# Kernel tuning notes

Measured on AMD Instinct MI355X. Metric: run time of the kernel, lower is better.

The kernel has to match this reference:

```python
import jax, jax.numpy as jnp
import numpy as np

B, N, IN_DIM, EMB, HEADS, M, ITERS = 8, 4096, 1024, 512, 4, 256, 6
DH = EMB // HEADS
SCALE = DH ** -0.5
RES_K = 33  # residual depthwise conv kernel size (TransMIL / nystrom-attention default)


def setup_inputs() -> dict:
    key = jax.random.key(0)
    ks = iter(jax.random.split(key, 40))
    def rn(shape, s=0.02):
        return jax.random.normal(next(ks), shape, jnp.float32) * s
    inp = {"X": jax.random.normal(next(ks), (B, N, IN_DIM), jnp.float32)}
    inp["few_w"] = rn((IN_DIM, EMB)); inp["few_b"] = jnp.zeros((EMB,), jnp.float32)
    inp["cls_token"] = rn((1, 1, EMB), 1.0)
    for i in (1, 2):
        inp[f"l{i}_ln_g"] = jnp.ones((EMB,), jnp.float32)
        inp[f"l{i}_ln_b"] = jnp.zeros((EMB,), jnp.float32)
        inp[f"l{i}_qkv_w"] = rn((EMB, 3 * EMB))
        inp[f"l{i}_out_w"] = rn((EMB, EMB))
        inp[f"l{i}_out_b"] = jnp.zeros((EMB,), jnp.float32)
        inp[f"l{i}_res_k"] = rn((HEADS, 1, RES_K, 1))
    for ksz in (7, 5, 3):
        inp[f"ppeg_k{ksz}"] = rn((EMB, 1, ksz, ksz))
        inp[f"ppeg_b{ksz}"] = jnp.zeros((EMB,), jnp.float32)
    inp["norm_g"] = jnp.ones((EMB,), jnp.float32)
    inp["norm_b"] = jnp.zeros((EMB,), jnp.float32)
    inp["cls_w"] = rn((EMB, 1)); inp["cls_b"] = jnp.zeros((1,), jnp.float32)
    return inp


def _ln(x, g, b):
    mu = x.mean(-1, keepdims=True)
    var = x.var(-1, keepdims=True)
    return (x - mu) / jnp.sqrt(var + 1e-5) * g + b


def _pinv(x, iters):
    # Moore-Penrose iterative pseudo-inverse of (..., m, m)
    abs_x = jnp.abs(x)
    z = jnp.swapaxes(x, -1, -2) / (abs_x.sum(-1).max() * abs_x.sum(-2).max())
    I = jnp.eye(x.shape[-1], dtype=x.dtype)
    for _ in range(iters):
        xz = x @ z
        z = 0.25 * z @ (13 * I - xz @ (15 * I - xz @ (7 * I - xz)))
    return z


def _nystrom_layer(x, ln_g, ln_b, qkv_w, out_w, out_b, res_k):
    # pre-norm transformer layer with Nystrom attention + residual depthwise conv
    b, n, d = x.shape
    h = _ln(x, ln_g, ln_b)
    pad = (-n) % M  # left-pad so seq divisible by n_landmarks
    hp = jnp.pad(h, ((0, 0), (pad, 0), (0, 0)))
    n_p = n + pad
    q, k, v = jnp.split(hp @ qkv_w, 3, axis=-1)
    def to_heads(t):
        return t.reshape(b, n_p, HEADS, DH).transpose(0, 2, 1, 3)  # (b,h,n,dh)
    q, k, v = to_heads(q) * SCALE, to_heads(k), to_heads(v)
    l = n_p // M
    q_l = q.reshape(b, HEADS, M, l, DH).mean(3)  # landmark means
    k_l = k.reshape(b, HEADS, M, l, DH).mean(3)
    a1 = jax.nn.softmax(jnp.einsum('bhid,bhjd->bhij', q, k_l), -1)    # (b,h,n,m)
    a2 = jax.nn.softmax(jnp.einsum('bhid,bhjd->bhij', q_l, k_l), -1)  # (b,h,m,m)
    a3 = jax.nn.softmax(jnp.einsum('bhid,bhjd->bhij', q_l, k), -1)    # (b,h,m,n)
    out = a1 @ (_pinv(a2, ITERS) @ (a3 @ v))
    # residual depthwise conv over sequence, one channel per head
    res = jax.lax.conv_general_dilated(
        v, res_k, (1, 1), ((RES_K // 2, RES_K // 2), (0, 0)),
        dimension_numbers=('NCHW', 'OIHW', 'NCHW'), feature_group_count=HEADS)
    out = out + res
    out = out.transpose(0, 2, 1, 3).reshape(b, n_p, d) @ out_w + out_b
    return x + out[:, -n:]


def _dwconv(x, k, bias, pad):
    y = jax.lax.conv_general_dilated(
        x, k, (1, 1), ((pad, pad), (pad, pad)),
        dimension_numbers=('NCHW', 'OIHW', 'NCHW'), feature_group_count=EMB)
    return y + bias[None, :, None, None]


def _ppeg(x, H, W, k7, b7, k5, b5, k3, b3):
    b, _, c = x.shape
    cls_t, feat = x[:, :1], x[:, 1:]
    f = feat.transpose(0, 2, 1).reshape(b, c, H, W)
    y = f + _dwconv(f, k7, b7, 3) + _dwconv(f, k5, b5, 2) + _dwconv(f, k3, b3, 1)
    y = y.reshape(b, c, H * W).transpose(0, 2, 1)
    return jnp.concatenate([cls_t, y], axis=1)


def _forward(X, few_w, few_b, cls_token,
             l1_ln_g, l1_ln_b, l1_qkv_w, l1_out_w, l1_out_b, l1_res_k,
             l2_ln_g, l2_ln_b, l2_qkv_w, l2_out_w, l2_out_b, l2_res_k,
             ppeg_k7, ppeg_b7, ppeg_k5, ppeg_b5, ppeg_k3, ppeg_b3,
             norm_g, norm_b, cls_w, cls_b):
    b, bag = X.shape[0], X.shape[1]
    h = X @ few_w + few_b
    ps = int(np.ceil(np.sqrt(bag)))
    add = ps * ps - bag
    h = jnp.concatenate([h, h[:, :add]], axis=1)  # pad bag to perfect square
    h = jnp.concatenate([jnp.broadcast_to(cls_token, (b, 1, EMB)), h], axis=1)
    h = _nystrom_layer(h, l1_ln_g, l1_ln_b, l1_qkv_w, l1_out_w, l1_out_b, l1_res_k)
    h = _ppeg(h, ps, ps, ppeg_k7, ppeg_b7, ppeg_k5, ppeg_b5, ppeg_k3, ppeg_b3)
    h = _nystrom_layer(h, l2_ln_g, l2_ln_b, l2_qkv_w, l2_out_w, l2_out_b, l2_res_k)
    h = _ln(h, norm_g, norm_b)
    return (h[:, 0] @ cls_w + cls_b).squeeze(-1)  # (batch,) bag logits


def reference(X, few_w, few_b, cls_token,
              l1_ln_g, l1_ln_b, l1_qkv_w, l1_out_w, l1_out_b, l1_res_k,
              l2_ln_g, l2_ln_b, l2_qkv_w, l2_out_w, l2_out_b, l2_res_k,
              ppeg_k7, ppeg_b7, ppeg_k5, ppeg_b5, ppeg_k3, ppeg_b3,
              norm_g, norm_b, cls_w, cls_b):
    return _forward(X, few_w, few_b, cls_token,
                    l1_ln_g, l1_ln_b, l1_qkv_w, l1_out_w, l1_out_b, l1_res_k,
                    l2_ln_g, l2_ln_b, l2_qkv_w, l2_out_w, l2_out_b, l2_res_k,
                    ppeg_k7, ppeg_b7, ppeg_k5, ppeg_b5, ppeg_k3, ppeg_b3,
                    norm_g, norm_b, cls_w, cls_b)
```

## Files before the change

### kernel.cpp

```cpp
#include <hip/hip_runtime.h>

constexpr int BATCH = 8;
constexpr int NTOK  = 4097;
constexpr int NP    = 4352;
constexpr int PADR  = 255;
constexpr int EMBD  = 512;
constexpr int DHD   = 128;
constexpr int LSUB  = 17;
constexpr float SCALE_F = 0.08838834764831845f;

constexpr int PPS   = 72;
constexpr int PPLN  = 72 * 70;
constexpr long long TPAD_FLOATS = (long long)BATCH * EMBD * PPLN;

typedef unsigned short u16;
typedef short   s16x8 __attribute__((ext_vector_type(8)));
typedef u16     u16x4 __attribute__((ext_vector_type(4)));
typedef float   f32x4 __attribute__((ext_vector_type(4)));

__device__ __forceinline__ u16 f2bf(float x) {
    unsigned u = __float_as_uint(x);
    u += 0x7fffu + ((u >> 16) & 1u);
    return (u16)(u >> 16);
}
__device__ __forceinline__ float bf2f(u16 h) {
    return __uint_as_float(((unsigned)h) << 16);
}

__device__ __forceinline__ void gload16(const u16* gp, u16* lp) {
    __builtin_amdgcn_global_load_lds(
        (const __attribute__((address_space(1))) unsigned int*)gp,
        (__attribute__((address_space(3))) unsigned int*)lp,
        16, 0, 0);
}

__device__ __forceinline__ float block_sum256(float v) {
    __shared__ float tmp[4];
    __syncthreads();
#pragma unroll
    for (int off = 32; off > 0; off >>= 1) v += __shfl_down(v, off, 64);
    int t = threadIdx.x;
    if ((t & 63) == 0) tmp[t >> 6] = v;
    __syncthreads();
    return tmp[0] + tmp[1] + tmp[2] + tmp[3];
}

__device__ __forceinline__ float block_max256(float v) {
    __shared__ float tmp[4];
    __syncthreads();
#pragma unroll
    for (int off = 32; off > 0; off >>= 1) v = fmaxf(v, __shfl_down(v, off, 64));
    int t = threadIdx.x;
    if ((t & 63) == 0) tmp[t >> 6] = v;
    __syncthreads();
    return fmaxf(fmaxf(tmp[0], tmp[1]), fmaxf(tmp[2], tmp[3]));
}

struct GemmP {
    const float* A; const float* B; float* C; const float* bias;
    long long As1, As2, Bs1, Bs2, Cs1, Cs2;
    int Adiv, Bdiv, Cdiv;
    int Am, Bk, Bn, Cm, Arow, Crow;
    int M, N, K, nb;
    float alpha; int accum;
    float bdiagc; int btrans; float cdiagc; int ctrans;
};

constexpr int LDSTR = 40;
constexpr int AH = 0, AL = 2560, BHs = 5120, BLs = 7680;

__global__ __launch_bounds__(256) void gemm_k(GemmP p) {
    __shared__ u16 lds[10240];
    const int bz = blockIdx.z;
    const float* Ab = p.A + (long long)(bz / p.Adiv) * p.As1 + (long long)(bz % p.Adiv) * p.As2;
    const float* Bb = p.B + (long long)(bz / p.Bdiv) * p.Bs1 + (long long)(bz % p.Bdiv) * p.Bs2;
    float*       Cb = p.C + (long long)(bz / p.Cdiv) * p.Cs1 + (long long)(bz % p.Cdiv) * p.Cs2;
    const int m0 = blockIdx.y * 64, n0 = blockIdx.x * 64;
    const int t = threadIdx.x;
    const int wave = t >> 6, lane = t & 63;
    const int wm = (wave & 1) * 32, wn = (wave >> 1) * 32;
    const int quad = lane >> 4, l15 = lane & 15;

    f32x4 acc[2][2];
#pragma unroll
    for (int i = 0; i < 2; ++i)
#pragma unroll
        for (int j = 0; j < 2; ++j) acc[i][j] = (f32x4){0.f, 0.f, 0.f, 0.f};

    for (int k0 = 0; k0 < p.K; k0 += 32) {
        {
            const int ar = t >> 2, ac = (t & 3) * 8;
            float v[8];
            if (m0 + ar < p.M) {
                const float* s = Ab + (long long)(m0 + ar + p.Arow) * p.Am + (k0 + ac);
                float4 x0 = *(const float4*)s, x1 = *(const float4*)(s + 4);
                v[0] = x0.x; v[1] = x0.y; v[2] = x0.z; v[3] = x0.w;
                v[4] = x1.x; v[5] = x1.y; v[6] = x1.z; v[7] = x1.w;
            } else {
#pragma unroll
                for (int i = 0; i < 8; ++i) v[i] = 0.f;
            }
            u16 h[8], l[8];
#pragma unroll
            for (int i = 0; i < 8; ++i) { h[i] = f2bf(v[i]); l[i] = f2bf(v[i] - bf2f(h[i])); }
            const int off = ar * LDSTR + ac;
            u16x4 a0, a1, b0, b1;
#pragma unroll
            for (int i = 0; i < 4; ++i) { a0[i] = h[i]; a1[i] = h[i + 4]; b0[i] = l[i]; b1[i] = l[i + 4]; }
            *(u16x4*)&lds[AH + off] = a0; *(u16x4*)&lds[AH + off + 4] = a1;
            *(u16x4*)&lds[AL + off] = b0; *(u16x4*)&lds[AL + off + 4] = b1;
        }
        if (p.Bn == 1) {
            const int bk = t >> 3, n8 = (t & 7) * 8;
            const float* s = Bb + (long long)(k0 + bk) * p.Bk + (n0 + n8);
            float4 x0 = *(const float4*)s, x1 = *(const float4*)(s + 4);
            float v[8] = {x0.x, x0.y, x0.z, x0.w, x1.x, x1.y, x1.z, x1.w};
            if (p.btrans) {
                const int gk = k0 + bk;
#pragma unroll
                for (int i = 0; i < 8; ++i)
                    v[i] = (gk == n0 + n8 + i ? p.bdiagc : 0.f) - v[i];
            }
#pragma unroll
            for (int i = 0; i < 8; ++i) {
                int j = (i + (t & 7)) & 7;
                u16 h = f2bf(v[j]);
                lds[BHs + (n8 + j) * LDSTR + bk] = h;
                lds[BLs + (n8 + j) * LDSTR + bk] = f2bf(v[j] - bf2f(h));
            }
        } else {
            const int bn = t >> 2, k8 = (t & 3) * 8;
            const float* s = Bb + (long long)(n0 + bn) * p.Bn + (k0 + k8);
            float4 x0 = *(const float4*)s, x1 = *(const float4*)(s + 4);
            float v[8] = {x0.x, x0.y, x0.z, x0.w, x1.x, x1.y, x1.z, x1.w};
            u16 h[8], l[8];
#pragma unroll
            for (int i = 0; i < 8; ++i) { h[i] = f2bf(v[i]); l[i] = f2bf(v[i] - bf2f(h[i])); }
            const int off = bn * LDSTR + k8;
            u16x4 a0, a1, b0, b1;
#pragma unroll
            for (int i = 0; i < 4; ++i) { a0[i] = h[i]; a1[i] = h[i + 4]; b0[i] = l[i]; b1[i] = l[i + 4]; }
            *(u16x4*)&lds[BHs + off] = a0; *(u16x4*)&lds[BHs + off + 4] = a1;
            *(u16x4*)&lds[BLs + off] = b0; *(u16x4*)&lds[BLs + off + 4] = b1;
        }
        __syncthreads();

        s16x8 ah[2], al[2], bh[2], bl[2];
#pragma unroll
        for (int mi = 0; mi < 2; ++mi) {
            const int off = (wm + mi * 16 + l15) * LDSTR + quad * 8;
            u16x4 q0 = *(const u16x4*)&lds[AH + off], q1 = *(const u16x4*)&lds[AH + off + 4];
            u16x4 r0 = *(const u16x4*)&lds[AL + off], r1 = *(const u16x4*)&lds[AL + off + 4];
            s16x8 fh, fl;
#pragma unroll
            for (int i = 0; i < 4; ++i) { fh[i] = q0[i]; fh[i + 4] = q1[i]; fl[i] = r0[i]; fl[i + 4] = r1[i]; }
            ah[mi] = fh; al[mi] = fl;
        }
#pragma unroll
        for (int ni = 0; ni < 2; ++ni) {
            const int off = (wn + ni * 16 + l15) * LDSTR + quad * 8;
            u16x4 q0 = *(const u16x4*)&lds[BHs + off], q1 = *(const u16x4*)&lds[BHs + off + 4];
            u16x4 r0 = *(const u16x4*)&lds[BLs + off], r1 = *(const u16x4*)&lds[BLs + off + 4];
            s16x8 fh, fl;
#pragma unroll
            for (int i = 0; i < 4; ++i) { fh[i] = q0[i]; fh[i + 4] = q1[i]; fl[i] = r0[i]; fl[i + 4] = r1[i]; }
            bh[ni] = fh; bl[ni] = fl;
        }
#pragma unroll
        for (int mi = 0; mi < 2; ++mi)
#pragma unroll
            for (int ni = 0; ni < 2; ++ni) {
                acc[mi][ni] = __builtin_amdgcn_mfma_f32_16x16x32_bf16(ah[mi], bh[ni], acc[mi][ni], 0, 0, 0);
                acc[mi][ni] = __builtin_amdgcn_mfma_f32_16x16x32_bf16(ah[mi], bl[ni], acc[mi][ni], 0, 0, 0);
                acc[mi][ni] = __builtin_amdgcn_mfma_f32_16x16x32_bf16(al[mi], bh[ni], acc[mi][ni], 0, 0, 0);
            }
        __syncthreads();
    }

#pragma unroll
    for (int mi = 0; mi < 2; ++mi)
#pragma unroll
        for (int ni = 0; ni < 2; ++ni) {
            const int n = n0 + wn + ni * 16 + l15;
#pragma unroll
            for (int r = 0; r < 4; ++r) {
                const int m = m0 + wm + mi * 16 + quad * 4 + r;
                if (m >= p.M) continue;
                float v = p.alpha * acc[mi][ni][r];
                if (p.bias) v += p.bias[n];
                if (p.ctrans) v = (m == n ? p.cdiagc : 0.f) - v;
                float* dst = Cb + (long long)(m + p.Crow) * p.Cm + n;
                if (p.accum) *dst += v; else *dst = v;
            }
        }
}

struct SplitP {
    const float* src; u16* dh; u16* dl;
    long long s1, s2, rstride, dstride, total;
    int div, R, C8;
    float scale;
};
__global__ __launch_bounds__(256) void split_k(SplitP p) {
    long long idx = (long long)blockIdx.x * 256 + threadIdx.x;
    if (idx >= p.total) return;
    int c8 = (int)(idx % p.C8);
    long long tmp = idx / p.C8;
    int r  = (int)(tmp % p.R);
    int bz = (int)(tmp / p.R);
    const float* s = p.src + (long long)(bz / p.div) * p.s1 + (long long)(bz % p.div) * p.s2
                   + (long long)r * p.rstride + c8 * 8;
    float4 x0 = *(const float4*)s, x1 = *(const float4*)(s + 4);
    float v[8] = {x0.x, x0.y, x0.z, x0.w, x1.x, x1.y, x1.z, x1.w};
    s16x8 hv, lv;
#pragma unroll
    for (int i = 0; i < 8; ++i) {
        float sv = v[i] * p.scale;
        u16 h = f2bf(sv);
        hv[i] = (short)h;
        lv[i] = (short)f2bf(sv - bf2f(h));
    }
    long long doff = (long long)bz * p.dstride + (long long)r * (p.C8 * 8) + c8 * 8;
    *(s16x8*)&p.dh[doff] = hv;
    *(s16x8*)&p.dl[doff] = lv;
}

__global__ __launch_bounds__(256) void splitT_k(const float* __restrict__ src,
                                                u16* __restrict__ dh, u16* __restrict__ dl,
                                                int K, int N) {
    int idx = blockIdx.x * 256 + threadIdx.x;
    if (idx >= N * K) return;
    int n = idx / K, k = idx - n * K;
    float v = src[(long long)k * N + n];
    u16 h = f2bf(v);
    dh[idx] = h;
    dl[idx] = f2bf(v - bf2f(h));
}

struct GemmBtP {
    const u16 *Ah, *Al, *Bh, *Bl;
    float* C; const float* bias;
    long long Abs, Bbs, Cbs;
    int M, N, K, Cm, Crow, accum;
};

__global__ __launch_bounds__(512, 4) void gemm_bt_k(GemmBtP p) {
    __shared__ __align__(16) u16 lds[16384];
    const int bz = blockIdx.z;
    const u16* Ahb = p.Ah + (long long)bz * p.Abs;
    const u16* Alb = p.Al + (long long)bz * p.Abs;
    const u16* Bhb = p.Bh + (long long)bz * p.Bbs;
    const u16* Blb = p.Bl + (long long)bz * p.Bbs;
    float*     Cb  = p.C  + (long long)bz * p.Cbs;

    const int NX = gridDim.x;
    const int nwg = NX * gridDim.y;
    const int bid = blockIdx.y * NX + blockIdx.x;
    const int qq = nwg >> 3, rr = nwg & 7;
    const int xcd = bid & 7, loc = bid >> 3;
    const int nbid = (xcd < rr) ? (xcd * (qq + 1) + loc)
                                : (rr * (qq + 1) + (xcd - rr) * qq + loc);
    const int m0 = (nbid / NX) * 128, n0 = (nbid % NX) * 256;

    const int t = threadIdx.x;
    const int wave = t >> 6, lane = t & 63;
    const int wm = (wave & 1) * 64, wn = (wave >> 1) * 64;
    const int quad = lane >> 4, l15 = lane & 15;
    const int K = p.K;

    const int srow = 16 * wave + (lane >> 2);
    const int sga  = (m0 + srow < p.M) ? (m0 + srow) : (p.M - 1);
    const long long sbase = (long long)sga * K + (lane & 3) * 8;
    u16* ldsw = &lds[wave * 512];

    const long long bb0   = (long long)(n0 + wn + l15) * K + quad * 8;
    const long long bstep = 16LL * K;

    f32x4 acc[4][4];
#pragma unroll
    for (int i = 0; i < 4; ++i)
#pragma unroll
        for (int j = 0; j < 4; ++j) acc[i][j] = (f32x4){0.f, 0.f, 0.f, 0.f};

    gload16(Ahb + sbase, ldsw);
    gload16(Alb + sbase, ldsw + 4096);
    __syncthreads();

    const int nt = K >> 5;
    int cur = 0;
    for (int t0 = 0; t0 < nt; ++t0) {
        const int k0 = t0 << 5;
        s16x8 bh[4], bl[4];
#pragma unroll
        for (int ni = 0; ni < 4; ++ni) {
            const long long bo = bb0 + ni * bstep + k0;
            bh[ni] = *(const s16x8*)&Bhb[bo];
            bl[ni] = *(const s16x8*)&Blb[bo];
        }
        if (t0 + 1 < nt) {
            u16* dst = ldsw + (cur ^ 1) * 8192;
            gload16(Ahb + sbase + k0 + 32, dst);
            gload16(Alb + sbase + k0 + 32, dst + 4096);
        }
        const int bufo = cur * 8192;
#pragma unroll
        for (int mi = 0; mi < 4; ++mi) {
            const int off = bufo + (wm + mi * 16 + l15) * 32 + quad * 8;
            s16x8 ah = *(const s16x8*)&lds[off];
            s16x8 al = *(const s16x8*)&lds[off + 4096];
#pragma unroll
            for (int ni = 0; ni < 4; ++ni) {
                acc[mi][ni] = __builtin_amdgcn_mfma_f32_16x16x32_bf16(ah, bh[ni], acc[mi][ni], 0, 0, 0);
                acc[mi][ni] = __builtin_amdgcn_mfma_f32_16x16x32_bf16(ah, bl[ni], acc[mi][ni], 0, 0, 0);
                acc[mi][ni] = __builtin_amdgcn_mfma_f32_16x16x32_bf16(al, bh[ni], acc[mi][ni], 0, 0, 0);
            }
        }
        __syncthreads();
        cur ^= 1;
    }

#pragma unroll
    for (int mi = 0; mi < 4; ++mi)
#pragma unroll
        for (int ni = 0; ni < 4; ++ni) {
            const int n = n0 + wn + ni * 16 + l15;
            const float bv = p.bias ? p.bias[n] : 0.f;
#pragma unroll
            for (int r = 0; r < 4; ++r) {
                const int m = m0 + wm + mi * 16 + quad * 4 + r;
                if (m >= p.M) continue;
                float* dst = Cb + (long long)(m + p.Crow) * p.Cm + n;
                float v = acc[mi][ni][r] + bv;
                if (p.accum) *dst += v; else *dst = v;
            }
        }
}

__global__ void cls_set_k(float* H0, const float* cls) {
    int t = blockIdx.x * 256 + threadIdx.x;
    int b = t >> 9, c = t & 511;
    H0[(long long)b * NTOK * EMBD + c] = cls[c];
}

__global__ __launch_bounds__(256) void ln_pad_k(const float* __restrict__ H0,
                                                u16* __restrict__ oh, u16* __restrict__ ol,
                                                const float* g, const float* bb) {
    int row = blockIdx.x, b = blockIdx.y, t = threadIdx.x;
    long long off = ((long long)b * NP + row) * EMBD;
    if (row < PADR) {
        oh[off + t] = 0; oh[off + t + 256] = 0;
        ol[off + t] = 0; ol[off + t + 256] = 0;
        return;
    }
    const float* x = H0 + ((long long)b * NTOK + (row - PADR)) * EMBD;
    float v0 = x[t], v1 = x[t + 256];
    float mu = block_sum256(v0 + v1) * (1.f / EMBD);
    float d0 = v0 - mu, d1 = v1 - mu;
    float var = block_sum256(d0 * d0 + d1 * d1) * (1.f / EMBD);
    float rs = 1.f / sqrtf(var + 1e-5f);
    float y0 = d0 * rs * g[t]       + bb[t];
    float y1 = d1 * rs * g[t + 256] + bb[t + 256];
    u16 h0 = f2bf(y0); oh[off + t]       = h0; ol[off + t]       = f2bf(y0 - bf2f(h0));
    u16 h1 = f2bf(y1); oh[off + t + 256] = h1; ol[off + t + 256] = f2bf(y1 - bf2f(h1));
}

__global__ void landmark_k(const float* __restrict__ QKV, float* __restrict__ QL,
                           float* __restrict__ KL) {
    long long idx = (long long)blockIdx.x * 256 + threadIdx.x;
    int d = idx & 127; int i = (int)((idx >> 7) & 255); int bh = (int)(idx >> 15);
    int b = bh >> 2, h = bh & 3;
    const float* base = QKV + (long long)b * NP * 1536 + (long long)i * LSUB * 1536 + h * DHD + d;
    float sq = 0.f, sk = 0.f;
#pragma unroll
    for (int j = 0; j < LSUB; ++j) { sq += base[j * 1536]; sk += base[j * 1536 + EMBD]; }
    QL[idx] = sq * (1.f / LSUB);
    KL[idx] = sk * (1.f / LSUB);
}

__global__ __launch_bounds__(256) void softmax256_k(float* __restrict__ X) {
    long long row = (long long)blockIdx.x * 4 + (threadIdx.x >> 6);
    int lane = threadIdx.x & 63;
    float4* p = (float4*)(X + row * 256) + lane;
    float4 v = *p;
    float m = fmaxf(fmaxf(v.x, v.y), fmaxf(v.z, v.w));
#pragma unroll
    for (int off = 32; off > 0; off >>= 1) m = fmaxf(m, __shfl_xor(m, off, 64));
    float ex = __expf(v.x - m), ey = __expf(v.y - m), ez = __expf(v.z - m), ew = __expf(v.w - m);
    float s = ex + ey + ez + ew;
#pragma unroll
    for (int off = 32; off > 0; off >>= 1) s += __shfl_xor(s, off, 64);
    float inv = 1.f / s;
    *p = make_float4(ex * inv, ey * inv, ez * inv, ew * inv);
}

__global__ __launch_bounds__(256) void softmax_k(float* __restrict__ X, int L) {
    float4* p = (float4*)(X + (long long)blockIdx.x * L);
    int nv = L >> 2, t = threadIdx.x;
    float m = -1e30f;
    for (int i = t; i < nv; i += 256) {
        float4 v = p[i];
        m = fmaxf(m, fmaxf(fmaxf(v.x, v.y), fmaxf(v.z, v.w)));
    }
    m = block_max256(m);
    float s = 0.f;
    for (int i = t; i < nv; i += 256) {
        float4 v = p[i];
        v.x = __expf(v.x - m); v.y = __expf(v.y - m); v.z = __expf(v.z - m); v.w = __expf(v.w - m);
        p[i] = v;
        s += v.x + v.y + v.z + v.w;
    }
    s = block_sum256(s);
    float inv = 1.f / s;
    for (int i = t; i < nv; i += 256) {
        float4 v = p[i];
        p[i] = make_float4(v.x * inv, v.y * inv, v.z * inv, v.w * inv);
    }
}

__global__ __launch_bounds__(256) void pinv_absmax_k(const float* __restrict__ X, float* red) {
    int bh = blockIdx.x, t = threadIdx.x;
    const float* x = X + (long long)bh * 65536;
    float rs = 0.f, cs = 0.f;
    for (int j = 0; j < 256; ++j) { rs += fabsf(x[t * 256 + j]); cs += fabsf(x[j * 256 + t]); }
    float mr = block_max256(rs);
    float mc = block_max256(cs);
    if (t == 0) { red[bh] = mr; red[32 + bh] = mc; }
}

__global__ void pinv_scalar_k(const float* red, float* inv) {
    float mr = 0.f, mc = 0.f;
    for (int i = 0; i < 32; ++i) { mr = fmaxf(mr, red[i]); mc = fmaxf(mc, red[32 + i]); }
    inv[0] = 1.f / (mr * mc);
}

__global__ void pinv_tinit_k(const float* __restrict__ X, const float* __restrict__ inv,
                             float* __restrict__ Z) {
    long long idx = (long long)blockIdx.x * 256 + threadIdx.x;
    int j = (int)(idx & 255); int i = (int)((idx >> 8) & 255); long long bh = idx >> 16;
    Z[idx] = X[(bh << 16) + ((long long)j << 8) + i] * inv[0];
}

__global__ void resconv_k(const float* __restrict__ QKV, const float* __restrict__ rk,
                          float* __restrict__ ATT2) {
    long long idx = (long long)blockIdx.x * 256 + threadIdx.x;
    if (idx >= (long long)BATCH * NTOK * EMBD) return;
    int c = (int)(idx & 511); long long r = idx >> 9;
    int n = PADR + (int)(r % NTOK); int b = (int)(r / NTOK);
    int h = c >> 7, d = c & 127;
    const float* vb = QKV + (long long)b * NP * 1536 + 1024 + h * DHD + d;
    float acc = 0.f;
#pragma unroll
    for (int u = 0; u < 33; ++u) {
        int nn = n + u - 16;
        if (nn >= 0 && nn < NP) acc += vb[(long long)nn * 1536] * rk[h * 33 + u];
    }
    ATT2[((long long)b * NP + n) * EMBD + c] += acc;
}

__global__ void wsum_k(const float* __restrict__ k7, const float* __restrict__ k5,
                       const float* __restrict__ k3, const float* __restrict__ b7,
                       const float* __restrict__ b5, const float* __restrict__ b3,
                       float* __restrict__ W) {
    int idx = blockIdx.x * 256 + threadIdx.x;
    if (idx < 25088) {
        int c = idx / 49, i = idx - c * 49;
        int dy = i / 7, dx = i - dy * 7;
        float w = k7[idx];
        if (dy >= 1 && dy <= 5 && dx >= 1 && dx <= 5) w += k5[c * 25 + (dy - 1) * 5 + (dx - 1)];
        if (dy >= 2 && dy <= 4 && dx >= 2 && dx <= 4) w += k3[c * 9 + (dy - 2) * 3 + (dx - 2)];
        W[idx] = w;
    } else if (idx < 25600) {
        int c = idx - 25088;
        W[25088 + c] = b7[c] + b5[c] + b3[c];
    }
}

__global__ __launch_bounds__(256) void tin_k(const float* __restrict__ H0,
                                             float* __restrict__ Tpad) {
    __shared__ float lds[64][65];
    const int y = blockIdx.x, c0 = blockIdx.y * 64, b = blockIdx.z;
    const int t = threadIdx.x;
    const int pc = t & 63, pr4 = t >> 6;
    const float* src = H0 + ((long long)b * NTOK + 1 + y * 64) * EMBD + c0;
#pragma unroll
    for (int i = 0; i < 16; ++i) {
        int pr = pr4 + i * 4;
        lds[pr][pc] = src[(long long)pr * EMBD + pc];
    }
    __syncthreads();
    const int xw = t & 63, cw4 = t >> 6;
#pragma unroll
    for (int i = 0; i < 16; ++i) {
        int cw = cw4 + i * 4;
        Tpad[(long long)(b * 512 + c0 + cw) * PPLN + (3 + y) * PPS + 3 + xw] = lds[xw][cw];
    }
}

__global__ __launch_bounds__(256, 4) void conv7_k(const float* __restrict__ Tpad,
                                                  const float* __restrict__ Wall,
                                                  float* __restrict__ Tout) {
    const int bc = blockIdx.x;
    const int c = bc & 511;
    const int t = threadIdx.x;
    const int x = t & 63, band = t >> 6;
    const int y0 = band * 16;
    const float* in = Tpad + (long long)bc * PPLN + x;
    float* outp = Tout + (long long)bc * 4096 + x;

    float W[49];
#pragma unroll
    for (int i = 0; i < 49; ++i) W[i] = Wall[c * 49 + i];
    const float bias = Wall[25088 + c];

    float win[7][7];
#pragma unroll
    for (int j = 0; j < 6; ++j)
#pragma unroll
        for (int d = 0; d < 7; ++d)
            win[j][d] = in[(y0 + j) * PPS + d];

#pragma unroll
    for (int yy = 0; yy < 16; ++yy) {
        const int slot = (6 + yy) % 7;
#pragma unroll
        for (int d = 0; d < 7; ++d)
            win[slot][d] = in[(y0 + yy + 6) * PPS + d];
        float s = bias + win[(yy + 3) % 7][3];
#pragma unroll
        for (int dy = 0; dy < 7; ++dy) {
            const int r = (yy + dy) % 7;
#pragma unroll
            for (int dx = 0; dx < 7; ++dx)
                s += W[dy * 7 + dx] * win[r][dx];
        }
        outp[(y0 + yy) * 64] = s;
    }
}

__global__ __launch_bounds__(256) void tout_k(const float* __restrict__ Tout,
                                              float* __restrict__ H0) {
    __shared__ float lds[64][65];
    const int y = blockIdx.x, c0 = blockIdx.y * 64, b = blockIdx.z;
    const int t = threadIdx.x;
    const int xl = t & 63, cl4 = t >> 6;
#pragma unroll
    for (int i = 0; i < 16; ++i) {
        int cl = cl4 + i * 4;
        lds[xl][cl] = Tout[(long long)(b * 512 + c0 + cl) * 4096 + y * 64 + xl];
    }
    __syncthreads();
    const int pc = t & 63, pl4 = t >> 6;
    float* dst = H0 + ((long long)b * NTOK + 1 + y * 64) * EMBD + c0;
#pragma unroll
    for (int i = 0; i < 16; ++i) {
        int pl = pl4 + i * 4;
        dst[(long long)pl * EMBD + pc] = lds[pl][pc];
    }
}

__global__ __launch_bounds__(256) void head_k(const float* __restrict__ H0, const float* g,
                                              const float* bb, const float* cw, const float* cb,
                                              float* __restrict__ out) {
    int b = blockIdx.x, t = threadIdx.x;
    const float* x = H0 + (long long)b * NTOK * EMBD;
    float v0 = x[t], v1 = x[t + 256];
    float mu = block_sum256(v0 + v1) * (1.f / EMBD);
    float d0 = v0 - mu, d1 = v1 - mu;
    float var = block_sum256(d0 * d0 + d1 * d1) * (1.f / EMBD);
    float rs = 1.f / sqrtf(var + 1e-5f);
    float y0 = d0 * rs * g[t] + bb[t];
    float y1 = d1 * rs * g[t + 256] + bb[t + 256];
    float s = block_sum256(y0 * cw[t] + y1 * cw[t + 256]);
    if (t == 0) out[b] = s + cb[0];
}

extern "C" void kernel_launch(void* const* d_in, const int* in_sizes, int n_in,
                              void* d_out, int out_size, void* d_ws, size_t ws_size,
                              hipStream_t stream) {
    (void)in_sizes; (void)n_in; (void)out_size; (void)ws_size;
    const float* X        = (const float*)d_in[0];
    const float* few_w    = (const float*)d_in[1];
    const float* few_b    = (const float*)d_in[2];
    const float* cls_tok  = (const float*)d_in[3];
    const float* ln_g[2]  = {(const float*)d_in[4],  (const float*)d_in[10]};
    const float* ln_b[2]  = {(const float*)d_in[5],  (const float*)d_in[11]};
    const float* qkv_w[2] = {(const float*)d_in[6],  (const float*)d_in[12]};
    const float* out_w[2] = {(const float*)d_in[7],  (const float*)d_in[13]};
    const float* out_b[2] = {(const float*)d_in[8],  (const float*)d_in[14]};
    const float* res_k[2] = {(const float*)d_in[9],  (const float*)d_in[15]};
    const float* k7 = (const float*)d_in[16]; const float* b7 = (const float*)d_in[17];
    const float* k5 = (const float*)d_in[18]; const float* b5 = (const float*)d_in[19];
    const float* k3 = (const float*)d_in[20]; const float* b3 = (const float*)d_in[21];
    const float* norm_g = (const float*)d_in[22]; const float* norm_b = (const float*)d_in[23];
    const float* cls_w  = (const float*)d_in[24]; const float* cls_b  = (const float*)d_in[25];
    float* out = (float*)d_out;

    float* ws  = (float*)d_ws;
    float* H0  = ws;
    float* LNH = H0  + 16781312LL;
    float* QKV = LNH + 17825792LL;
    float* A3  = QKV + 53477376LL;
    float* QL  = A3  + 35651584LL;
    float* KL  = QL  + 1048576LL;
    float* A2  = KL  + 1048576LL;
    float* KV  = A2  + 2097152LL;
    float* ZKV = KV  + 1048576LL;
    float* RED = ZKV + 1048576LL;

    u16* LNHh = (u16*)LNH;
    u16* LNHl = (u16*)(LNH + 8912896LL);
    u16* QLh  = (u16*)KV;
    u16* QLl  = (u16*)(KV + 524288LL);
    u16* KLh  = (u16*)ZKV;
    u16* KLl  = (u16*)(ZKV + 524288LL);
    u16* Xh   = (u16*)A3;
    u16* Xl   = (u16*)(A3 + 16777216LL);
    u16* ATh  = (u16*)A3;
    u16* ATl  = (u16*)(A3 + 8390656LL);
    u16* Wh   = (u16*)A2;
    u16* fwl  = (u16*)(A2 + 262144LL);
    u16* qwl  = (u16*)(A2 + 393216LL);
    u16* owl  = (u16*)(A2 + 131072LL);
    float* Zb0 = LNH;
    float* Zb1 = LNH + 2097152LL;
    float* XZm = LNH + 4194304LL;
    float* U1  = LNH + 6291456LL;
    float* U2  = LNH + 8388608LL;
    float* Tpad = QKV;
    float* Tout = QKV + TPAD_FLOATS;
    float* WSUM = A3;

    auto gemmx = [&](const float* A, long long As1, long long As2, int Adiv, int Am, int Arow,
                     const float* Bm, long long Bs1, long long Bs2, int Bdiv, int Bk, int Bn,
                     float* C, long long Cs1, long long Cs2, int Cdiv, int Cm, int Crow,
                     int M, int N, int K, int nb, float alpha, int accum, const float* bias,
                     float bdiagc, int btrans, float cdiagc, int ctrans) {
        GemmP p;
        p.A = A; p.B = Bm; p.C = C; p.bias = bias;
        p.As1 = As1; p.As2 = As2; p.Bs1 = Bs1; p.Bs2 = Bs2; p.Cs1 = Cs1; p.Cs2 = Cs2;
        p.Adiv = Adiv; p.Bdiv = Bdiv; p.Cdiv = Cdiv;
        p.Am = Am; p.Bk = Bk; p.Bn = Bn; p.Cm = Cm; p.Arow = Arow; p.Crow = Crow;
        p.M = M; p.N = N; p.K = K; p.nb = nb; p.alpha = alpha; p.accum = accum;
        p.bdiagc = bdiagc; p.btrans = btrans; p.cdiagc = cdiagc; p.ctrans = ctrans;
        dim3 grid(N / 64, (M + 63) / 64, nb);
        gemm_k<<<grid, 256, 0, stream>>>(p);
    };
    auto gemm = [&](const float* A, long long As1, long long As2, int Adiv, int Am, int Arow,
                    const float* Bm, long long Bs1, long long Bs2, int Bdiv, int Bk, int Bn,
                    float* C, long long Cs1, long long Cs2, int Cdiv, int Cm, int Crow,
                    int M, int N, int K, int nb, float alpha, int accum, const float* bias) {
        gemmx(A, As1, As2, Adiv, Am, Arow, Bm, Bs1, Bs2, Bdiv, Bk, Bn,
              C, Cs1, Cs2, Cdiv, Cm, Crow, M, N, K, nb, alpha, accum, bias, 0.f, 0, 0.f, 0);
    };
    auto split = [&](const float* src, u16* dh, u16* dl, long long s1, long long s2, int div,
                     long long rstride, int R, int C, int nb, float scale) {
        SplitP p;
        p.src = src; p.dh = dh; p.dl = dl;
        p.s1 = s1; p.s2 = s2; p.div = div;
        p.rstride = rstride; p.R = R; p.C8 = C >> 3;
        p.dstride = (long long)R * C;
        p.total = (long long)nb * R * (C >> 3);
        p.scale = scale;
        int blocks = (int)((p.total + 255) / 256);
        split_k<<<blocks, 256, 0, stream>>>(p);
    };
    auto gemmbt = [&](const u16* Ah, const u16* Al, long long Abs,
                      const u16* Bh, const u16* Bl, long long Bbs,
                      float* C, long long Cbs, int Cm, int Crow,
                      int M, int N, int K, int nb, int accum, const float* bias) {
        GemmBtP p;
        p.Ah = Ah; p.Al = Al; p.Bh = Bh; p.Bl = Bl;
        p.C = C; p.bias = bias;
        p.Abs = Abs; p.Bbs = Bbs; p.Cbs = Cbs;
        p.M = M; p.N = N; p.K = K; p.Cm = Cm; p.Crow = Crow; p.accum = accum;
        dim3 grid(N / 256, (M + 127) / 128, nb);
        gemm_bt_k<<<grid, 512, 0, stream>>>(p);
    };

    cls_set_k<<<16, 256, 0, stream>>>(H0, cls_tok);
    split(X, Xh, Xl, 0, 0, 1, 1024, 32768, 1024, 1, 1.f);
    splitT_k<<<2048, 256, 0, stream>>>(few_w, Wh, fwl, 1024, 512);
    gemmbt(Xh, Xl, 4194304LL, Wh, fwl, 0,
           H0, 2097664LL, 512, 1,
           4096, 512, 1024, BATCH, 0, few_b);

    for (int L = 0; L < 2; ++L) {
        ln_pad_k<<<dim3(NP, BATCH), 256, 0, stream>>>(H0, LNHh, LNHl, ln_g[L], ln_b[L]);
        splitT_k<<<3072, 256, 0, stream>>>(qkv_w[L], Wh, qwl, 512, 1536);
        gemmbt(LNHh, LNHl, 0, Wh, qwl, 0,
               QKV, 0, 1536, 0,
               34816, 1536, 512, 1, 0, nullptr);
        landmark_k<<<4096, 256, 0, stream>>>(QKV, QL, KL);
        gemm(QL, 32768LL, 0, 1, 128, 0,
             KL, 32768LL, 0, 1, 1, 128,
             A2, 65536LL, 0, 1, 256, 0,
             256, 256, 128, 32, SCALE_F, 0, nullptr);
        softmax256_k<<<2048, 256, 0, stream>>>(A2);
        split(QL, QLh, QLl, 32768LL, 0, 1, 128, 256, 128, 32, SCALE_F);
        split(KL, KLh, KLl, 32768LL, 0, 1, 128, 256, 128, 32, 1.f);
        split(QKV + 512, LNHh, LNHl, 6680064LL, 128LL, 4, 1536, 4352, 128, 32, 1.f);
        gemmbt(QLh, QLl, 32768LL, LNHh, LNHl, 557056LL,
               A3, 1114112LL, 4352, 0,
               256, 4352, 128, 32, 0, nullptr);
        softmax_k<<<8192, 256, 0, stream>>>(A3, 4352);
        gemm(A3, 1114112LL, 0, 1, 4352, 0,
             QKV + 1024, 6680064LL, 128LL, 4, 1536, 1,
             KV, 32768LL, 0, 1, 128, 0,
             256, 128, 4352, 32, 1.f, 0, nullptr);
        split(QKV, LNHh, LNHl, 6680064LL, 128LL, 4, 1536, 4352, 128, 32, SCALE_F);
        gemmbt(LNHh, LNHl, 557056LL, KLh, KLl, 32768LL,
               A3, 1114112LL, 256, 0,
               4352, 256, 128, 32, 0, nullptr);
        softmax256_k<<<34816, 256, 0, stream>>>(A3);
        pinv_absmax_k<<<32, 256, 0, stream>>>(A2, RED);
        pinv_scalar_k<<<1, 1, 0, stream>>>(RED, RED + 64);
        pinv_tinit_k<<<8192, 256, 0, stream>>>(A2, RED + 64, Zb0);
        float* zc = Zb0; float* zn = Zb1;
        for (int it = 0; it < 6; ++it) {
            gemm(A2, 65536LL, 0, 1, 256, 0, zc, 65536LL, 0, 1, 256, 1,
                 XZm, 65536LL, 0, 1, 256, 0, 256, 256, 256, 32, 1.f, 0, nullptr);
            gemmx(XZm, 65536LL, 0, 1, 256, 0, XZm, 65536LL, 0, 1, 256, 1,
                  U1, 65536LL, 0, 1, 256, 0, 256, 256, 256, 32, 1.f, 0, nullptr,
                  7.f, 1, 15.f, 1);
            gemmx(XZm, 65536LL, 0, 1, 256, 0, U1, 65536LL, 0, 1, 256, 1,
                  U2, 65536LL, 0, 1, 256, 0, 256, 256, 256, 32, 1.f, 0, nullptr,
                  0.f, 0, 13.f, 1);
            gemm(zc, 65536LL, 0, 1, 256, 0, U2, 65536LL, 0, 1, 256, 1,
                 zn, 65536LL, 0, 1, 256, 0, 256, 256, 256, 32, 0.25f, 0, nullptr);
            float* t2 = zc; zc = zn; zn = t2;
        }
        gemm(zc, 65536LL, 0, 1, 256, 0,
             KV, 32768LL, 0, 1, 128, 1,
             ZKV, 32768LL, 0, 1, 128, 0,
             256, 128, 256, 32, 1.f, 0, nullptr);
        gemm(A3, 1114112LL, 0, 1, 256, 0,
             ZKV, 32768LL, 0, 1, 128, 1,
             LNH, 2228224LL, 128LL, 4, 512, 0,
             4352, 128, 256, 32, 1.f, 0, nullptr);
        resconv_k<<<65552, 256, 0, stream>>>(QKV, res_k[L], LNH);
        split(LNH + PADR * 512, ATh, ATl, 2228224LL, 0, 1, 512, 4097, 512, 8, 1.f);
        splitT_k<<<1024, 256, 0, stream>>>(out_w[L], Wh, owl, 512, 512);
        gemmbt(ATh, ATl, 2097664LL, Wh, owl, 0,
               H0, 2097664LL, 512, 0,
               4097, 512, 512, BATCH, 1, out_b[L]);

        if (L == 0) {
            hipMemsetAsync(Tpad, 0, TPAD_FLOATS * sizeof(float), stream);
            wsum_k<<<101, 256, 0, stream>>>(k7, k5, k3, b7, b5, b3, WSUM);
            tin_k<<<dim3(64, 8, 8), 256, 0, stream>>>(H0, Tpad);
            conv7_k<<<4096, 256, 0, stream>>>(Tpad, WSUM, Tout);
            tout_k<<<dim3(64, 8, 8), 256, 0, stream>>>(Tout, H0);
        }
    }

    head_k<<<BATCH, 256, 0, stream>>>(H0, norm_g, norm_b, cls_w, cls_b, out);
}
```

Measured before the change: 4.372 ms.

## Deepen gemm_bt K-tile to 64 with XOR-swizzled LDS; cache softmax rows in LDS

The split-bf16 GEMM (B-transposed) now stages 64-wide K tiles instead of 32. The A tile goes into an LDS buffer twice as large, with an XOR swizzle on the 8-element column chunks to avoid bank conflicts, and B fragments are loaded per 32-wide half. This halves the number of barriers and loop iterations per K. The long-row softmax (L=4352) now keeps the row in shared memory, so global memory is read once and written once instead of three reads and two writes. The larger LDS footprint (64KB for the GEMM, about 17KB for the softmax) may reduce occupancy.

```diff
diff --git a/kernel.cpp b/kernel.cpp
--- a/kernel.cpp
+++ b/kernel.cpp
@@ -245,7 +245,7 @@
 };
 
 __global__ __launch_bounds__(512, 4) void gemm_bt_k(GemmBtP p) {
-    __shared__ __align__(16) u16 lds[16384];
+    __shared__ __align__(16) u16 lds[32768];
     const int bz = blockIdx.z;
     const u16* Ahb = p.Ah + (long long)bz * p.Abs;
     const u16* Alb = p.Al + (long long)bz * p.Abs;
@@ -268,10 +268,14 @@
     const int quad = lane >> 4, l15 = lane & 15;
     const int K = p.K;
 
-    const int srow = 16 * wave + (lane >> 2);
-    const int sga  = (m0 + srow < p.M) ? (m0 + srow) : (p.M - 1);
-    const long long sbase = (long long)sga * K + (lane & 3) * 8;
-    u16* ldsw = &lds[wave * 512];
+    const int lrow = lane >> 3;
+    const int jx   = (lane & 7) ^ lrow;
+    const int r0   = wave * 16 + lrow;
+    const int sga0 = (m0 + r0     < p.M) ? (m0 + r0)     : (p.M - 1);
+    const int sga1 = (m0 + r0 + 8 < p.M) ? (m0 + r0 + 8) : (p.M - 1);
+    const long long sb0 = (long long)sga0 * K + jx * 8;
+    const long long sb1 = (long long)sga1 * K + jx * 8;
+    u16* ldsw = &lds[wave * 1024];
 
     const long long bb0   = (long long)(n0 + wn + l15) * K + quad * 8;
     const long long bstep = 16LL * K;
@@ -282,37 +286,45 @@
 #pragma unroll
         for (int j = 0; j < 4; ++j) acc[i][j] = (f32x4){0.f, 0.f, 0.f, 0.f};
 
-    gload16(Ahb + sbase, ldsw);
-    gload16(Alb + sbase, ldsw + 4096);
+    auto STAGE = [&](int buf, int ko) {
+        u16* d = ldsw + buf * 16384;
+        gload16(Ahb + sb0 + ko, d);
+        gload16(Ahb + sb1 + ko, d + 512);
+        gload16(Alb + sb0 + ko, d + 8192);
+        gload16(Alb + sb1 + ko, d + 8192 + 512);
+    };
+
+    STAGE(0, 0);
     __syncthreads();
 
-    const int nt = K >> 5;
+    const int nt = K >> 6;
     int cur = 0;
     for (int t0 = 0; t0 < nt; ++t0) {
-        const int k0 = t0 << 5;
-        s16x8 bh[4], bl[4];
-#pragma unroll
-        for (int ni = 0; ni < 4; ++ni) {
-            const long long bo = bb0 + ni * bstep + k0;
-            bh[ni] = *(const s16x8*)&Bhb[bo];
-            bl[ni] = *(const s16x8*)&Blb[bo];
-        }
-        if (t0 + 1 < nt) {
-            u16* dst = ldsw + (cur ^ 1) * 8192;
-            gload16(Ahb + sbase + k0 + 32, dst);
-            gload16(Alb + sbase + k0 + 32, dst + 4096);
-        }
-        const int bufo = cur * 8192;
-#pragma unroll
-        for (int mi = 0; mi < 4; ++mi) {
-            const int off = bufo + (wm + mi * 16 + l15) * 32 + quad * 8;
-            s16x8 ah = *(const s16x8*)&lds[off];
-            s16x8 al = *(const s16x8*)&lds[off + 4096];
+        const int k0 = t0 << 6;
+        if (t0 + 1 < nt) STAGE(cur ^ 1, k0 + 64);
+        const int bufo = cur * 16384;
+#pragma unroll
+        for (int kh = 0; kh < 2; ++kh) {
+            s16x8 bh[4], bl[4];
 #pragma unroll
             for (int ni = 0; ni < 4; ++ni) {
-                acc[mi][ni] = __builtin_amdgcn_mfma_f32_16x16x32_bf16(ah, bh[ni], acc[mi][ni], 0, 0, 0);
-                acc[mi][ni] = __builtin_amdgcn_mfma_f32_16x16x32_bf16(ah, bl[ni], acc[mi][ni], 0, 0, 0);
-                acc[mi][ni] = __builtin_amdgcn_mfma_f32_16x16x32_bf16(al, bh[ni], acc[mi][ni], 0, 0, 0);
+                const long long bo = bb0 + ni * bstep + k0 + kh * 32;
+                bh[ni] = *(const s16x8*)&Bhb[bo];
+                bl[ni] = *(const s16x8*)&Blb[bo];
+            }
+#pragma unroll
+            for (int mi = 0; mi < 4; ++mi) {
+                const int r  = wm + mi * 16 + l15;
+                const int c8 = kh * 4 + quad;
+                const int off = bufo + r * 64 + ((c8 ^ (r & 7)) << 3);
+                s16x8 ah = *(const s16x8*)&lds[off];
+                s16x8 al = *(const s16x8*)&lds[off + 8192];
+#pragma unroll
+                for (int ni = 0; ni < 4; ++ni) {
+                    acc[mi][ni] = __builtin_amdgcn_mfma_f32_16x16x32_bf16(ah, bh[ni], acc[mi][ni], 0, 0, 0);
+                    acc[mi][ni] = __builtin_amdgcn_mfma_f32_16x16x32_bf16(ah, bl[ni], acc[mi][ni], 0, 0, 0);
+                    acc[mi][ni] = __builtin_amdgcn_mfma_f32_16x16x32_bf16(al, bh[ni], acc[mi][ni], 0, 0, 0);
+                }
             }
         }
         __syncthreads();
@@ -393,26 +405,28 @@
     *p = make_float4(ex * inv, ey * inv, ez * inv, ew * inv);
 }
 
-__global__ __launch_bounds__(256) void softmax_k(float* __restrict__ X, int L) {
-    float4* p = (float4*)(X + (long long)blockIdx.x * L);
-    int nv = L >> 2, t = threadIdx.x;
+__global__ __launch_bounds__(256) void softmax_lds_k(float* __restrict__ X) {
+    __shared__ float rowbuf[4352];
+    float4* p  = (float4*)(X + (long long)blockIdx.x * 4352);
+    float4* r4 = (float4*)rowbuf;
+    const int t = threadIdx.x;
     float m = -1e30f;
-    for (int i = t; i < nv; i += 256) {
-        float4 v = p[i];
+    for (int i = t; i < 1088; i += 256) {
+        float4 v = p[i]; r4[i] = v;
         m = fmaxf(m, fmaxf(fmaxf(v.x, v.y), fmaxf(v.z, v.w)));
     }
     m = block_max256(m);
     float s = 0.f;
-    for (int i = t; i < nv; i += 256) {
-        float4 v = p[i];
+    for (int i = t; i < 1088; i += 256) {
+        float4 v = r4[i];
         v.x = __expf(v.x - m); v.y = __expf(v.y - m); v.z = __expf(v.z - m); v.w = __expf(v.w - m);
-        p[i] = v;
+        r4[i] = v;
         s += v.x + v.y + v.z + v.w;
     }
     s = block_sum256(s);
     float inv = 1.f / s;
-    for (int i = t; i < nv; i += 256) {
-        float4 v = p[i];
+    for (int i = t; i < 1088; i += 256) {
+        float4 v = r4[i];
         p[i] = make_float4(v.x * inv, v.y * inv, v.z * inv, v.w * inv);
     }
 }
@@ -702,7 +716,7 @@
         gemmbt(QLh, QLl, 32768LL, LNHh, LNHl, 557056LL,
                A3, 1114112LL, 4352, 0,
                256, 4352, 128, 32, 0, nullptr);
-        softmax_k<<<8192, 256, 0, stream>>>(A3, 4352);
+        softmax_lds_k<<<8192, 256, 0, stream>>>(A3);
         gemm(A3, 1114112LL, 0, 1, 4352, 0,
              QKV + 1024, 6680064LL, 128LL, 4, 1536, 1,
              KV, 32768LL, 0, 1, 128, 0,
```

Result: slower. 4.493 ms (+2.8%).
